# Optimization experiments

Hardware: AMD Instinct MI355X
Metric: run time of the kernel (lower is better)

Reference implementation:

```python
import jax, jax.numpy as jnp
import numpy as np

HIDDEN = 512
SCALE = 1.0 / np.sqrt(HIDDEN).astype(np.float32)
MASK_FILL = -1e20


def setup_inputs() -> dict:
    key = jax.random.key(0)
    k1, k2 = jax.random.split(key)
    B, S, D = 4, 4096, HIDDEN
    X = jax.random.normal(k1, (B, S, D), dtype=jnp.float32)
    W = jax.random.normal(k2, (D, 3 * D), dtype=jnp.float32) * (1.0 / np.sqrt(D))
    b = jnp.zeros((3 * D,), dtype=jnp.float32)
    attention_mask = jnp.ones((B, 1, S), dtype=jnp.int32)
    return {"X": X, "W": W, "b": b, "attention_mask": attention_mask}


def reference(X, W, b, attention_mask):
    # fused QKV projection: [B,S,3D]
    QKV = jnp.einsum('bsd,de->bse', X, W) + b
    Q, K, V = jnp.split(QKV, 3, axis=-1)
    # full score matrix [B,S,S] (the memory-bound part)
    scores = jnp.einsum('bqd,bkd->bqk', Q, K)
    # faithful: mask BEFORE scaling (fill value also gets divided by sqrt(d))
    scores = jnp.where(attention_mask == 0, MASK_FILL, scores)
    attn = jax.nn.softmax(scores * SCALE, axis=-1)
    # dropout disabled (eval mode) for deterministic reference
    out = jnp.einsum('bqk,bkd->bqd', attn, V)
    return out
```

## Files before the change

kernel.cpp:

```cpp
#include <hip/hip_runtime.h>
#include <cstdint>

#define B_  4
#define S_  4096
#define D_  512

#define SCALEF 0.04419417382415922f
#define QSF    0.06375885f
#define MASK_FILLF -1e20f
#define MASKQ  -6.375885e18f
#define FMAX2  17.312340f

typedef __attribute__((ext_vector_type(8))) short b16x8;
typedef __attribute__((ext_vector_type(4))) float f32x4;
typedef __attribute__((ext_vector_type(16))) float f32x16;

__device__ __forceinline__ unsigned short f2bf(float f) {
    unsigned int u = __builtin_bit_cast(unsigned int, f);
    u += 0x7fffu + ((u >> 16) & 1u);
    return (unsigned short)(u >> 16);
}

__device__ __forceinline__ float exp2fast(float x) {
#if __has_builtin(__builtin_amdgcn_exp2f)
    return __builtin_amdgcn_exp2f(x);
#else
    return __expf(x * 0.69314718056f);
#endif
}

__device__ __forceinline__ void gl_lds16(const void* gp, void* lp) {
    __builtin_amdgcn_global_load_lds(
        (const __attribute__((address_space(1))) unsigned int*)(uintptr_t)gp,
        (__attribute__((address_space(3))) unsigned int*)(uintptr_t)lp,
        16, 0, 0);
}

__global__ __launch_bounds__(256) void cast_fused_kernel(
    const float* __restrict__ X, unsigned short* __restrict__ Xb,
    const float* __restrict__ W, unsigned short* __restrict__ Wt) {
    __shared__ float t[32][33];
    int bid = blockIdx.x;
    if (bid < 8192) {
        int i = (bid * 256 + threadIdx.x) * 4;
        float4 v = *(const float4*)(X + i);
        ushort4 o;
        o.x = f2bf(v.x); o.y = f2bf(v.y); o.z = f2bf(v.z); o.w = f2bf(v.w);
        *(ushort4*)(Xb + i) = o;
    } else {
        int bb = bid - 8192;
        int tx = threadIdx.x & 31, ty0 = threadIdx.x >> 5;
        int e0 = (bb % 48) * 32;
        int d0 = (bb / 48) * 32;
#pragma unroll
        for (int p = 0; p < 4; ++p) {
            int ty = ty0 + p * 8;
            t[ty][tx] = W[(size_t)(d0 + ty) * 1536 + e0 + tx];
        }
        __syncthreads();
#pragma unroll
        for (int p = 0; p < 4; ++p) {
            int ty = ty0 + p * 8;
            Wt[(size_t)(e0 + ty) * 512 + d0 + tx] = f2bf(t[tx][ty]);
        }
    }
}

__global__ __launch_bounds__(256) void qkv_gemm_kernel(
    const unsigned short* __restrict__ Xb, const unsigned short* __restrict__ Wt,
    const float* __restrict__ bias,
    unsigned short* __restrict__ Qb, unsigned short* __restrict__ Kb,
    unsigned short* __restrict__ Vt) {
    __shared__ char lds[32768];
    const int tid = threadIdx.x, lane = tid & 63, wave = tid >> 6;
    const int quad = lane >> 4, kcol = lane & 15;
    const int wm = wave & 1, wn = wave >> 1;
    const int lin = blockIdx.x;
    const int xcd = lin & 7;
    const int j = lin >> 3;
    const int bx = (j & 15) * 8 + xcd;
    const int by = j >> 4;
    const int row0 = bx * 128;
    const int col0 = by * 128;

    unsigned agl[2], bgl[2], lloc[2];
#pragma unroll
    for (int i = 0; i < 2; ++i) {
        int L = (wave * 2 + i) * 64 + lane;
        int r = L >> 2;
        int c = (L & 3) ^ ((r >> 1) & 3);
        agl[i] = (unsigned)((row0 + r) * 1024 + c * 16);
        bgl[i] = (unsigned)((col0 + r) * 1024 + c * 16);
        lloc[i] = (unsigned)(((wave * 2 + i) * 64) * 16);
    }

    f32x4 acc[4][4];
#pragma unroll
    for (int mt = 0; mt < 4; ++mt)
#pragma unroll
        for (int nt = 0; nt < 4; ++nt) acc[mt][nt] = (f32x4){0.f, 0.f, 0.f, 0.f};

    auto stage = [&](int kk) {
        char* la = lds + (kk & 1) * 16384;
        char* lb = la + 8192;
#pragma unroll
        for (int i = 0; i < 2; ++i) {
            gl_lds16((const char*)Xb + agl[i] + kk * 64, la + lloc[i]);
            gl_lds16((const char*)Wt + bgl[i] + kk * 64, lb + lloc[i]);
        }
    };

    stage(0);
    for (int kk = 0; kk < 16; ++kk) {
        __syncthreads();
        if (kk < 15) stage(kk + 1);
        const char* la = lds + (kk & 1) * 16384;
        const char* lb = la + 8192;
        b16x8 af[4], bfr[4];
#pragma unroll
        for (int mt = 0; mt < 4; ++mt) {
            int rr = wm * 64 + mt * 16 + kcol;
            af[mt] = *(const b16x8*)(la + rr * 64 + ((quad ^ ((rr >> 1) & 3)) << 4));
        }
#pragma unroll
        for (int nt = 0; nt < 4; ++nt) {
            int rr = wn * 64 + nt * 16 + kcol;
            bfr[nt] = *(const b16x8*)(lb + rr * 64 + ((quad ^ ((rr >> 1) & 3)) << 4));
        }
#pragma unroll
        for (int mt = 0; mt < 4; ++mt)
#pragma unroll
            for (int nt = 0; nt < 4; ++nt)
                acc[mt][nt] = __builtin_amdgcn_mfma_f32_16x16x32_bf16(af[mt], bfr[nt], acc[mt][nt], 0, 0, 0);
    }

    const int colbase = col0 + wn * 64;
    const int sec = colbase >> 9;
    const int cbase = colbase & 511;
    float bv[4];
#pragma unroll
    for (int nt = 0; nt < 4; ++nt) bv[nt] = bias[colbase + nt * 16 + kcol];

    if (sec < 2) {
        unsigned short* dst = sec == 0 ? Qb : Kb;
        const float scl = sec == 0 ? QSF : 1.0f;
#pragma unroll
        for (int mt = 0; mt < 4; ++mt) {
            int rg0 = row0 + wm * 64 + mt * 16 + quad * 4;
#pragma unroll
            for (int r = 0; r < 4; ++r) {
                size_t rowoff = (size_t)(rg0 + r) * 512;
#pragma unroll
                for (int nt = 0; nt < 4; ++nt)
                    dst[rowoff + cbase + nt * 16 + kcol] = f2bf((acc[mt][nt][r] + bv[nt]) * scl);
            }
        }
    } else {
#pragma unroll
        for (int mt = 0; mt < 4; ++mt) {
            int g0 = row0 + wm * 64 + mt * 16 + quad * 4;
#pragma unroll
            for (int r = 0; r < 4; ++r) {
                int g = g0 + r;
                int s = g & 4095;
                size_t pbase = (((size_t)(g >> 12) * 128 + (s >> 5)) << 14) + (s & 31);
#pragma unroll
                for (int nt = 0; nt < 4; ++nt) {
                    int d = cbase + nt * 16 + kcol;
                    Vt[pbase + (size_t)d * 32] = f2bf(acc[mt][nt][r] + bv[nt]);
                }
            }
        }
    }
}

__global__ __launch_bounds__(384, 2) void flash_kernel(
    const unsigned short* __restrict__ Qb, const unsigned short* __restrict__ Kb,
    const unsigned short* __restrict__ Vt, const int* __restrict__ maskG,
    float* __restrict__ Out) {
    extern __shared__ char smem[];
    const int tid = threadIdx.x;
    const int lane = tid & 63;
    const int wave = tid >> 6;
    const int lin = blockIdx.x;
    const int b = lin & 3;
    const int qrow0 = (lin >> 2) * 64;
    const int NI = 64;

    char* ldsK = smem;
    unsigned short* Pb = (unsigned short*)(smem + 131072);
    float* lbuf = (float*)Pb;

    const char* kgbase = (const char*)(Kb + (size_t)b * S_ * D_);
    const char* vgbase = (const char*)Vt + (size_t)b * 128 * 32768;
    const int* mrow = maskG + b * S_;

    if (wave < 2) {
        const int keyrow = lane & 31;
        const int hh = lane >> 5;
        const int swz = lane & 7;

        b16x8 qf[32];
        {
            const unsigned short* qptr =
                Qb + (size_t)(b * S_ + qrow0 + wave * 32 + keyrow) * D_ + hh * 8;
#pragma unroll
            for (int ks = 0; ks < 32; ++ks) qf[ks] = *(const b16x8*)(qptr + ks * 16);
        }
        float lsum16[16];
#pragma unroll
        for (int r = 0; r < 16; ++r) lsum16[r] = 0.f;

        for (int it = 0; it < NI; ++it) {
            __syncthreads();
            const char* kl = ldsK + (it & 1) * 65536;
            unsigned short* Ppar = Pb + (it & 1) * 5120;
#pragma unroll
            for (int h = 0; h < 2; ++h) {
                const bool um = mrow[it * 64 + h * 32 + keyrow] != 0;
                f32x16 sA, sB;
#pragma unroll
                for (int i = 0; i < 16; ++i) { sA[i] = 0.f; sB[i] = 0.f; }
#pragma unroll
                for (int ks = 0; ks < 32; ++ks) {
                    b16x8 kf = *(const b16x8*)(kl + (h * 32 + keyrow) * 1024 +
                                               (((ks * 2 + hh) ^ swz) << 4));
                    if (ks & 1) sB = __builtin_amdgcn_mfma_f32_32x32x16_bf16(qf[ks], kf, sB, 0, 0, 0);
                    else        sA = __builtin_amdgcn_mfma_f32_32x32x16_bf16(qf[ks], kf, sA, 0, 0, 0);
                }
                unsigned short* Pcur = Ppar + h * 2560;
#pragma unroll
                for (int r = 0; r < 16; ++r) {
                    float sv = sA[r] + sB[r];
                    float lg = um ? sv : MASKQ;
                    float ex = exp2fast(lg - FMAX2);
                    lsum16[r] += ex;
                    int row = (r & 3) + 8 * (r >> 2) + 4 * hh + wave * 32;
                    Pcur[row * 40 + keyrow] = f2bf(ex);
                }
            }
        }
        __syncthreads();

#pragma unroll
        for (int r = 0; r < 16; ++r) {
            float l = lsum16[r];
            l += __shfl_xor(l, 1);
            l += __shfl_xor(l, 2);
            l += __shfl_xor(l, 4);
            l += __shfl_xor(l, 8);
            l += __shfl_xor(l, 16);
            if ((lane & 31) == 0) {
                int row = (r & 3) + 8 * (r >> 2) + 4 * hh + wave * 32;
                lbuf[row] = 1.0f / l;
            }
        }
        __syncthreads();
    } else {
        const int ws = wave - 2;
        const int dw = ws * 128;
        const int quad = lane >> 4;
        const int kcol = lane & 15;

        unsigned kgl[16], kll[16];
#pragma unroll
        for (int i = 0; i < 16; ++i) {
            int r = ws * 16 + i;
            kgl[i] = (unsigned)(r * 1024 + (lane ^ (r & 7)) * 16);
            kll[i] = (unsigned)(r * 1024);
        }

        f32x4 o[4][8];
#pragma unroll
        for (int m = 0; m < 4; ++m)
#pragma unroll
            for (int n = 0; n < 8; ++n) o[m][n] = (f32x4){0.f, 0.f, 0.f, 0.f};

        {
#pragma unroll
            for (int i = 0; i < 16; ++i) gl_lds16(kgbase + kgl[i], ldsK + kll[i]);
        }

        for (int it = 0; it < NI; ++it) {
            __syncthreads();

            b16x8 vf[8], pf[4];
            const unsigned short* Ppar = Pb + ((it ^ 1) & 1) * 5120;
            if (it > 0) {
                const char* vtile = vgbase + (size_t)((it - 1) * 2) * 32768;
#pragma unroll
                for (int n = 0; n < 8; ++n)
                    vf[n] = *(const b16x8*)(vtile + (size_t)(dw + n * 16 + kcol) * 64 + quad * 16);
#pragma unroll
                for (int m = 0; m < 4; ++m)
                    pf[m] = *(const b16x8*)((const char*)Ppar + (m * 16 + kcol) * 80 + quad * 16);
            }

            if (it + 1 < NI) {
                const char* kg = kgbase + (size_t)(it + 1) * 65536;
                char* kl2 = ldsK + ((it + 1) & 1) * 65536;
#pragma unroll
                for (int i = 0; i < 16; ++i) gl_lds16(kg + kgl[i], kl2 + kll[i]);
            }

            if (it > 0) {
#pragma unroll
                for (int m = 0; m < 4; ++m)
#pragma unroll
                    for (int n = 0; n < 8; ++n)
                        o[m][n] = __builtin_amdgcn_mfma_f32_16x16x32_bf16(pf[m], vf[n], o[m][n], 0, 0, 0);

                const char* vtileb = vgbase + (size_t)((it - 1) * 2 + 1) * 32768;
#pragma unroll
                for (int n = 0; n < 8; ++n)
                    vf[n] = *(const b16x8*)(vtileb + (size_t)(dw + n * 16 + kcol) * 64 + quad * 16);
                const unsigned short* Pcb = Ppar + 2560;
#pragma unroll
                for (int m = 0; m < 4; ++m)
                    pf[m] = *(const b16x8*)((const char*)Pcb + (m * 16 + kcol) * 80 + quad * 16);
#pragma unroll
                for (int m = 0; m < 4; ++m)
#pragma unroll
                    for (int n = 0; n < 8; ++n)
                        o[m][n] = __builtin_amdgcn_mfma_f32_16x16x32_bf16(pf[m], vf[n], o[m][n], 0, 0, 0);
            }
        }
        __syncthreads();

        {
            const unsigned short* Ppar = Pb + ((NI - 1) & 1) * 5120;
#pragma unroll
            for (int h = 0; h < 2; ++h) {
                const char* vtile = vgbase + (size_t)((NI - 1) * 2 + h) * 32768;
                b16x8 vf[8], pf[4];
#pragma unroll
                for (int n = 0; n < 8; ++n)
                    vf[n] = *(const b16x8*)(vtile + (size_t)(dw + n * 16 + kcol) * 64 + quad * 16);
                const unsigned short* Pcur = Ppar + h * 2560;
#pragma unroll
                for (int m = 0; m < 4; ++m)
                    pf[m] = *(const b16x8*)((const char*)Pcur + (m * 16 + kcol) * 80 + quad * 16);
#pragma unroll
                for (int m = 0; m < 4; ++m)
#pragma unroll
                    for (int n = 0; n < 8; ++n)
                        o[m][n] = __builtin_amdgcn_mfma_f32_16x16x32_bf16(pf[m], vf[n], o[m][n], 0, 0, 0);
            }
        }
        __syncthreads();

#pragma unroll
        for (int m = 0; m < 4; ++m) {
            f32x4 lv = *(const f32x4*)(lbuf + m * 16 + quad * 4);
#pragma unroll
            for (int r = 0; r < 4; ++r) {
                size_t off = ((size_t)b * S_ + qrow0 + m * 16 + quad * 4 + r) * D_ + dw + kcol;
#pragma unroll
                for (int n = 0; n < 8; ++n) Out[off + n * 16] = o[m][n][r] * lv[r];
            }
        }
    }
}

extern "C" void kernel_launch(void* const* d_in, const int* in_sizes, int n_in,
                              void* d_out, int out_size, void* d_ws, size_t ws_size,
                              hipStream_t stream) {
    const float* X = (const float*)d_in[0];
    const float* W = (const float*)d_in[1];
    const float* bias = (const float*)d_in[2];
    const int* mask = (const int*)d_in[3];
    float* out = (float*)d_out;

    char* w = (char*)d_ws;
    unsigned short* Xb = (unsigned short*)w;  w += (size_t)16384 * 512 * 2;
    unsigned short* Wt = (unsigned short*)w;  w += (size_t)1536 * 512 * 2;
    unsigned short* Qb = (unsigned short*)w;  w += (size_t)16384 * 512 * 2;
    unsigned short* Kb = (unsigned short*)w;  w += (size_t)16384 * 512 * 2;
    unsigned short* Vt = (unsigned short*)w;  w += (size_t)16384 * 512 * 2;

    cast_fused_kernel<<<8960, 256, 0, stream>>>(X, Xb, W, Wt);
    qkv_gemm_kernel<<<1536, 256, 0, stream>>>(Xb, Wt, bias, Qb, Kb, Vt);

    (void)hipFuncSetAttribute((const void*)flash_kernel,
                              hipFuncAttributeMaxDynamicSharedMemorySize, 151552);
    flash_kernel<<<256, 384, 151552, stream>>>(Qb, Kb, Vt, mask, out);
}
```

Baseline: 311.0 us.

## Read K directly from global in a fragment-packed layout instead of LDS staging

The QKV GEMM now writes K in a tiled, MFMA-fragment-packed layout, so the score waves load K fragments straight from global/L2 with coalesced 16-byte reads. This removes the double-buffered 128 KB LDS staging of K that the PV waves used to issue. Dynamic shared memory drops to 20 KB, holding only the P buffers. The trade-off is that each of the two score waves now reads K from global/L2 with no sharing through LDS, which adds latency and cache traffic on the critical QK path.

```diff
diff --git a/kernel.cpp b/kernel.cpp
--- a/kernel.cpp
+++ b/kernel.cpp
@@ -69,7 +69,7 @@
 __global__ __launch_bounds__(256) void qkv_gemm_kernel(
     const unsigned short* __restrict__ Xb, const unsigned short* __restrict__ Wt,
     const float* __restrict__ bias,
-    unsigned short* __restrict__ Qb, unsigned short* __restrict__ Kb,
+    unsigned short* __restrict__ Qb, unsigned short* __restrict__ Kp,
     unsigned short* __restrict__ Vt) {
     __shared__ char lds[32768];
     const int tid = threadIdx.x, lane = tid & 63, wave = tid >> 6;
@@ -141,9 +141,7 @@
 #pragma unroll
     for (int nt = 0; nt < 4; ++nt) bv[nt] = bias[colbase + nt * 16 + kcol];
 
-    if (sec < 2) {
-        unsigned short* dst = sec == 0 ? Qb : Kb;
-        const float scl = sec == 0 ? QSF : 1.0f;
+    if (sec == 0) {
 #pragma unroll
         for (int mt = 0; mt < 4; ++mt) {
             int rg0 = row0 + wm * 64 + mt * 16 + quad * 4;
@@ -152,7 +150,25 @@
                 size_t rowoff = (size_t)(rg0 + r) * 512;
 #pragma unroll
                 for (int nt = 0; nt < 4; ++nt)
-                    dst[rowoff + cbase + nt * 16 + kcol] = f2bf((acc[mt][nt][r] + bv[nt]) * scl);
+                    Qb[rowoff + cbase + nt * 16 + kcol] = f2bf((acc[mt][nt][r] + bv[nt]) * QSF);
+            }
+        }
+    } else if (sec == 1) {
+#pragma unroll
+        for (int mt = 0; mt < 4; ++mt) {
+            int g0 = row0 + wm * 64 + mt * 16 + quad * 4;
+#pragma unroll
+            for (int r = 0; r < 4; ++r) {
+                int g = g0 + r;
+                int s = g & 4095;
+                size_t pbase = ((size_t)((g >> 12) * 128 + (s >> 5))) * 32768 +
+                               (size_t)(s & 31) * 16;
+#pragma unroll
+                for (int nt = 0; nt < 4; ++nt) {
+                    int d = cbase + nt * 16 + kcol;
+                    *(unsigned short*)((char*)Kp + pbase + (d >> 3) * 512 + (d & 7) * 2) =
+                        f2bf(acc[mt][nt][r] + bv[nt]);
+                }
             }
         }
     } else {
@@ -175,7 +191,7 @@
 }
 
 __global__ __launch_bounds__(384, 2) void flash_kernel(
-    const unsigned short* __restrict__ Qb, const unsigned short* __restrict__ Kb,
+    const unsigned short* __restrict__ Qb, const unsigned short* __restrict__ Kp,
     const unsigned short* __restrict__ Vt, const int* __restrict__ maskG,
     float* __restrict__ Out) {
     extern __shared__ char smem[];
@@ -187,18 +203,16 @@
     const int qrow0 = (lin >> 2) * 64;
     const int NI = 64;
 
-    char* ldsK = smem;
-    unsigned short* Pb = (unsigned short*)(smem + 131072);
-    float* lbuf = (float*)Pb;
-
-    const char* kgbase = (const char*)(Kb + (size_t)b * S_ * D_);
+    unsigned short* Pb = (unsigned short*)smem;
+    float* lbuf = (float*)smem;
+
+    const char* kpbase = (const char*)Kp + (size_t)b * 128 * 32768;
     const char* vgbase = (const char*)Vt + (size_t)b * 128 * 32768;
     const int* mrow = maskG + b * S_;
 
     if (wave < 2) {
         const int keyrow = lane & 31;
         const int hh = lane >> 5;
-        const int swz = lane & 7;
 
         b16x8 qf[32];
         {
@@ -213,18 +227,17 @@
 
         for (int it = 0; it < NI; ++it) {
             __syncthreads();
-            const char* kl = ldsK + (it & 1) * 65536;
             unsigned short* Ppar = Pb + (it & 1) * 5120;
 #pragma unroll
             for (int h = 0; h < 2; ++h) {
                 const bool um = mrow[it * 64 + h * 32 + keyrow] != 0;
+                const char* ktile = kpbase + (size_t)(it * 2 + h) * 32768;
                 f32x16 sA, sB;
 #pragma unroll
                 for (int i = 0; i < 16; ++i) { sA[i] = 0.f; sB[i] = 0.f; }
 #pragma unroll
                 for (int ks = 0; ks < 32; ++ks) {
-                    b16x8 kf = *(const b16x8*)(kl + (h * 32 + keyrow) * 1024 +
-                                               (((ks * 2 + hh) ^ swz) << 4));
+                    b16x8 kf = *(const b16x8*)(ktile + (ks * 2 + hh) * 512 + keyrow * 16);
                     if (ks & 1) sB = __builtin_amdgcn_mfma_f32_32x32x16_bf16(qf[ks], kf, sB, 0, 0, 0);
                     else        sA = __builtin_amdgcn_mfma_f32_32x32x16_bf16(qf[ks], kf, sA, 0, 0, 0);
                 }
@@ -262,31 +275,18 @@
         const int quad = lane >> 4;
         const int kcol = lane & 15;
 
-        unsigned kgl[16], kll[16];
-#pragma unroll
-        for (int i = 0; i < 16; ++i) {
-            int r = ws * 16 + i;
-            kgl[i] = (unsigned)(r * 1024 + (lane ^ (r & 7)) * 16);
-            kll[i] = (unsigned)(r * 1024);
-        }
-
         f32x4 o[4][8];
 #pragma unroll
         for (int m = 0; m < 4; ++m)
 #pragma unroll
             for (int n = 0; n < 8; ++n) o[m][n] = (f32x4){0.f, 0.f, 0.f, 0.f};
-
-        {
-#pragma unroll
-            for (int i = 0; i < 16; ++i) gl_lds16(kgbase + kgl[i], ldsK + kll[i]);
-        }
 
         for (int it = 0; it < NI; ++it) {
             __syncthreads();
 
-            b16x8 vf[8], pf[4];
-            const unsigned short* Ppar = Pb + ((it ^ 1) & 1) * 5120;
             if (it > 0) {
+                const unsigned short* Ppar = Pb + ((it ^ 1) & 1) * 5120;
+                b16x8 vf[8], pf[4];
                 const char* vtile = vgbase + (size_t)((it - 1) * 2) * 32768;
 #pragma unroll
                 for (int n = 0; n < 8; ++n)
@@ -294,16 +294,6 @@
 #pragma unroll
                 for (int m = 0; m < 4; ++m)
                     pf[m] = *(const b16x8*)((const char*)Ppar + (m * 16 + kcol) * 80 + quad * 16);
-            }
-
-            if (it + 1 < NI) {
-                const char* kg = kgbase + (size_t)(it + 1) * 65536;
-                char* kl2 = ldsK + ((it + 1) & 1) * 65536;
-#pragma unroll
-                for (int i = 0; i < 16; ++i) gl_lds16(kg + kgl[i], kl2 + kll[i]);
-            }
-
-            if (it > 0) {
 #pragma unroll
                 for (int m = 0; m < 4; ++m)
 #pragma unroll
@@ -375,13 +365,13 @@
     unsigned short* Xb = (unsigned short*)w;  w += (size_t)16384 * 512 * 2;
     unsigned short* Wt = (unsigned short*)w;  w += (size_t)1536 * 512 * 2;
     unsigned short* Qb = (unsigned short*)w;  w += (size_t)16384 * 512 * 2;
-    unsigned short* Kb = (unsigned short*)w;  w += (size_t)16384 * 512 * 2;
+    unsigned short* Kp = (unsigned short*)w;  w += (size_t)16384 * 512 * 2;
     unsigned short* Vt = (unsigned short*)w;  w += (size_t)16384 * 512 * 2;
 
     cast_fused_kernel<<<8960, 256, 0, stream>>>(X, Xb, W, Wt);
-    qkv_gemm_kernel<<<1536, 256, 0, stream>>>(Xb, Wt, bias, Qb, Kb, Vt);
+    qkv_gemm_kernel<<<1536, 256, 0, stream>>>(Xb, Wt, bias, Qb, Kp, Vt);
 
     (void)hipFuncSetAttribute((const void*)flash_kernel,
-                              hipFuncAttributeMaxDynamicSharedMemorySize, 151552);
-    flash_kernel<<<256, 384, 151552, stream>>>(Qb, Kb, Vt, mask, out);
-}
+                              hipFuncAttributeMaxDynamicSharedMemorySize, 20480);
+    flash_kernel<<<256, 384, 20480, stream>>>(Qb, Kp, Vt, mask, out);
+}
```

After: 700.7 us. 125% more time.
